# Optimization experiments

Hardware: AMD Instinct MI355X
Metric: run time of the kernel (lower is better)

The kernel has to match this reference:

```python
import jax, jax.numpy as jnp
import numpy as np
from jax import lax


def setup_inputs() -> dict:
    key = jax.random.key(0)
    ks = jax.random.split(key, 6)
    B, L, D, H, K = 32, 256, 16, 64, 5
    T = L - K + 1            # 252
    S = (T // 2) * H         # 8064
    return {
        "x": jax.random.normal(ks[0], (B, L, D), dtype=jnp.float32),
        "conv_w": jax.random.normal(ks[1], (D, H, K), dtype=jnp.float32) * 0.1,
        "conv_b": jax.random.normal(ks[2], (D, H), dtype=jnp.float32) * 0.1,
        "deconv_w": jax.random.normal(ks[3], (D, H, K), dtype=jnp.float32) * 0.1,
        "deconv_b": jax.random.normal(ks[4], (D,), dtype=jnp.float32) * 0.1,
        "W_attn": jax.random.normal(ks[5], (S, S), dtype=jnp.float32) * 0.01,
    }


def reference(x, conv_w, conv_b, deconv_w, deconv_b, W_attn):
    B, L, D = x.shape
    _, H, K = conv_w.shape
    T = L - K + 1
    P = T // 2
    S = P * H

    xt = jnp.transpose(x, (0, 2, 1))  # [B, D, L]
    # per-channel Conv1d(1->H) as one grouped conv: kernel [D*H, 1, K], groups=D
    y = lax.conv_general_dilated(
        xt, conv_w.reshape(D * H, 1, K), (1,), "VALID",
        dimension_numbers=("NCH", "OIH", "NCH"), feature_group_count=D,
    ) + conv_b.reshape(1, D * H, 1)
    y = jax.nn.relu(y)  # [B, D*H, T]

    # per-channel ConvTranspose1d(H->1) == full conv with flipped kernel, groups=D
    recon = lax.conv_general_dilated(
        y, deconv_w[..., ::-1], (1,), [(K - 1, K - 1)],
        dimension_numbers=("NCH", "OIH", "NCH"), feature_group_count=D,
    ) + deconv_b.reshape(1, D, 1)  # [B, D, L]

    # AvgPool1d(kernel=2, stride=2) then flatten(H, P) per channel
    pooled = y.reshape(B, D, H, P, 2).mean(axis=-1)  # [B, D, H, P]
    flat = pooled.reshape(B, D, S)                   # [B, D, S]

    main = flat[:, 0]        # [B, S]
    aux = flat[:, 1:]        # [B, D-1, S]

    # 'general' score: main . (aux @ W^T)  ==  (main @ W) . aux
    m = main @ W_attn                              # [B, S]
    scores = jnp.einsum("bt,bdt->bd", m, aux)      # [B, D-1]
    attn = jax.nn.softmax(scores, axis=-1)         # [B, D-1]
    weighted = jnp.einsum("bd,bds->bs", attn, aux)  # [B, S]

    out = jnp.concatenate([main[:, None, :], weighted[:, None, :]], axis=2)  # [B,1,2S]
    return out, attn[:, None, :], recon
```

## Files before the change

### kernel.cpp

```cpp
#include <hip/hip_runtime.h>
#include <math.h>

#define BB 32
#define LL 256
#define DD 16
#define HH 64
#define KK 5
#define TT 252
#define PP 126
#define SS 8064
#define NCHUNK 21
#define CHUNK 384
#define NKT 12

typedef __attribute__((ext_vector_type(8))) short bf16x8;
typedef __attribute__((ext_vector_type(4))) float f32x4;

__device__ __forceinline__ unsigned short f2bf(float f) {
  unsigned int u = __float_as_uint(f);
  u += 0x7FFFu + ((u >> 16) & 1u);
  return (unsigned short)(u >> 16);
}
__device__ __forceinline__ float bf2f(unsigned short h) {
  return __uint_as_float(((unsigned int)h) << 16);
}

__global__ __launch_bounds__(256) void k12_conv_recon(
    const float* __restrict__ x, const float* __restrict__ cw,
    const float* __restrict__ cb, const float* __restrict__ dw,
    const float* __restrict__ db, float* __restrict__ flat,
    unsigned short* __restrict__ mainH, unsigned short* __restrict__ mainL,
    float* __restrict__ recon) {
  __shared__ float ylds[HH * TT];
  __shared__ float xs[LL];
  __shared__ float cws[HH * KK];
  __shared__ float dws[HH * KK];
  __shared__ float cbs[HH];

  int bd = blockIdx.x;
  int b = bd / DD, d = bd % DD;
  int tid = threadIdx.x;

  xs[tid] = x[((size_t)b * LL + tid) * DD + d];
  for (int i = tid; i < HH * KK; i += 256) {
    cws[i] = cw[(size_t)d * HH * KK + i];
    dws[i] = dw[(size_t)d * HH * KK + i];
  }
  if (tid < HH) cbs[tid] = cb[d * HH + tid];
  __syncthreads();

  {
    int h = tid >> 2, a = tid & 3;
    int t0 = a * 63;
    float w0 = cws[h * KK + 0], w1 = cws[h * KK + 1], w2 = cws[h * KK + 2],
          w3 = cws[h * KK + 3], w4 = cws[h * KK + 4];
    float bias = cbs[h];
    float x0 = xs[t0], x1 = xs[t0 + 1], x2 = xs[t0 + 2], x3 = xs[t0 + 3],
          x4 = xs[t0 + 4];
    float* yrow = ylds + h * TT + t0;
    #pragma unroll 7
    for (int t = 0; t < 63; ++t) {
      float yv = fmaf(w4, x4, fmaf(w3, x3, fmaf(w2, x2, fmaf(w1, x1, fmaf(w0, x0, bias)))));
      yrow[t] = fmaxf(yv, 0.f);
      x0 = x1; x1 = x2; x2 = x3; x3 = x4;
      if (t < 62) x4 = xs[t0 + t + 5];
    }
  }
  __syncthreads();

  for (int i = tid; i < HH * PP; i += 256) {
    int h = i / PP, p = i - h * PP;
    float pooled = 0.5f * (ylds[h * TT + 2 * p] + ylds[h * TT + 2 * p + 1]);
    flat[(size_t)bd * SS + i] = pooled;
    if (d == 0) {
      unsigned short hb = f2bf(pooled);
      mainH[(size_t)b * SS + i] = hb;
      mainL[(size_t)b * SS + i] = f2bf(pooled - bf2f(hb));
    }
  }

  {
    int l = tid;
    float acc = db[d];
    for (int h = 0; h < HH; ++h) {
      const float* yl = ylds + h * TT;
      #pragma unroll
      for (int j = 0; j < KK; ++j) {
        int t = l - j;
        if (t >= 0 && t < TT) acc = fmaf(yl[t], dws[h * KK + j], acc);
      }
    }
    recon[(size_t)bd * LL + l] = acc;
  }
}

__global__ __launch_bounds__(256) void k3_mfma(
    const float* __restrict__ W, const unsigned short* __restrict__ mainH,
    const unsigned short* __restrict__ mainL, float* __restrict__ partial) {
  __shared__ unsigned short AH[2][1024];
  __shared__ unsigned short AL[2][1024];
  __shared__ unsigned short BH[2][4096];

  int tid = threadIdx.x;
  int chunk = blockIdx.y;
  int s0 = chunk * CHUNK;
  int cbase = blockIdx.x * 128;

  int lane = tid & 63;
  int wv = tid >> 6;
  int mr = wv & 1;
  int ctb = (wv >> 1) * 4;

  f32x4 c0 = {0.f, 0.f, 0.f, 0.f};
  f32x4 c1 = {0.f, 0.f, 0.f, 0.f};
  f32x4 c2 = {0.f, 0.f, 0.f, 0.f};
  f32x4 c3 = {0.f, 0.f, 0.f, 0.f};

  int sc2 = (tid & 63) * 2;
  int sg = tid >> 6;
  const float* wbase = W + (size_t)(s0 + sg * 8) * SS + cbase + sc2;

  int ab = tid >> 2, aq = tid & 3;
  size_t abase = (size_t)ab * SS + (size_t)(s0 + aq * 8);

  int aoff  = (lane >> 4) * 256 + ((lane & 15) + 16 * mr) * 8;
  int boff0 = (lane >> 4) * 1024 + (ctb * 16 + (lane & 15)) * 8;

  float2 e0, e1, e2, e3, e4, e5, e6, e7;
  float2 o0, o1, o2, o3, o4, o5, o6, o7;
  bf16x8 aEH, aEL, aOH, aOL;

#define LOADW(R0,R1,R2,R3,R4,R5,R6,R7, KT) {                          \
    const float* p_ = wbase + (size_t)(KT) * 32 * SS;                 \
    R0 = *(const float2*)(p_);                                        \
    R1 = *(const float2*)(p_ + (size_t)SS);                           \
    R2 = *(const float2*)(p_ + 2 * (size_t)SS);                       \
    R3 = *(const float2*)(p_ + 3 * (size_t)SS);                       \
    R4 = *(const float2*)(p_ + 4 * (size_t)SS);                       \
    R5 = *(const float2*)(p_ + 5 * (size_t)SS);                       \
    R6 = *(const float2*)(p_ + 6 * (size_t)SS);                       \
    R7 = *(const float2*)(p_ + 7 * (size_t)SS); }

#define LOADA(RH, RL, KT) if (tid < 128) {                            \
    RH = *(const bf16x8*)(mainH + abase + (KT) * 32);                 \
    RL = *(const bf16x8*)(mainL + abase + (KT) * 32); }

#define CVT1(F, J) {                                                  \
    h0[J] = (short)f2bf(F.x);                                         \
    h1[J] = (short)f2bf(F.y); }

#define CVTW(R0,R1,R2,R3,R4,R5,R6,R7, BUF) {                          \
    bf16x8 h0, h1;                                                    \
    CVT1(R0, 0) CVT1(R1, 1) CVT1(R2, 2) CVT1(R3, 3)                   \
    CVT1(R4, 4) CVT1(R5, 5) CVT1(R6, 6) CVT1(R7, 7)                   \
    *(bf16x8*)&BH[BUF][sg * 1024 + sc2 * 8]     = h0;                 \
    *(bf16x8*)&BH[BUF][sg * 1024 + sc2 * 8 + 8] = h1; }

#define WRITEA(RH, RL, BUF) if (tid < 128) {                          \
    *(bf16x8*)&AH[BUF][aq * 256 + ab * 8] = RH;                       \
    *(bf16x8*)&AL[BUF][aq * 256 + ab * 8] = RL; }

#define DOMFMA(BUF) {                                                 \
    bf16x8 ah  = *(const bf16x8*)&AH[BUF][aoff];                      \
    bf16x8 al  = *(const bf16x8*)&AL[BUF][aoff];                      \
    bf16x8 bh0 = *(const bf16x8*)&BH[BUF][boff0];                     \
    bf16x8 bh1 = *(const bf16x8*)&BH[BUF][boff0 + 128];               \
    bf16x8 bh2 = *(const bf16x8*)&BH[BUF][boff0 + 256];               \
    bf16x8 bh3 = *(const bf16x8*)&BH[BUF][boff0 + 384];               \
    c0 = __builtin_amdgcn_mfma_f32_16x16x32_bf16(ah, bh0, c0, 0, 0, 0); \
    c0 = __builtin_amdgcn_mfma_f32_16x16x32_bf16(al, bh0, c0, 0, 0, 0); \
    c1 = __builtin_amdgcn_mfma_f32_16x16x32_bf16(ah, bh1, c1, 0, 0, 0); \
    c1 = __builtin_amdgcn_mfma_f32_16x16x32_bf16(al, bh1, c1, 0, 0, 0); \
    c2 = __builtin_amdgcn_mfma_f32_16x16x32_bf16(ah, bh2, c2, 0, 0, 0); \
    c2 = __builtin_amdgcn_mfma_f32_16x16x32_bf16(al, bh2, c2, 0, 0, 0); \
    c3 = __builtin_amdgcn_mfma_f32_16x16x32_bf16(ah, bh3, c3, 0, 0, 0); \
    c3 = __builtin_amdgcn_mfma_f32_16x16x32_bf16(al, bh3, c3, 0, 0, 0); }

  LOADW(e0,e1,e2,e3,e4,e5,e6,e7, 0) LOADA(aEH, aEL, 0)
  CVTW(e0,e1,e2,e3,e4,e5,e6,e7, 0) WRITEA(aEH, aEL, 0)
  LOADW(o0,o1,o2,o3,o4,o5,o6,o7, 1) LOADA(aOH, aOL, 1)
  __syncthreads();

  #pragma unroll 1
  for (int kt = 0; kt < NKT; kt += 2) {
    if (kt + 2 < NKT) { LOADW(e0,e1,e2,e3,e4,e5,e6,e7, kt + 2) LOADA(aEH, aEL, kt + 2) }
    DOMFMA(0)
    CVTW(o0,o1,o2,o3,o4,o5,o6,o7, 1) WRITEA(aOH, aOL, 1)
    __syncthreads();
    if (kt + 3 < NKT) { LOADW(o0,o1,o2,o3,o4,o5,o6,o7, kt + 3) LOADA(aOH, aOL, kt + 3) }
    DOMFMA(1)
    if (kt + 2 < NKT) { CVTW(e0,e1,e2,e3,e4,e5,e6,e7, 0) WRITEA(aEH, aEL, 0) }
    __syncthreads();
  }

  int row0 = mr * 16 + (lane >> 4) * 4;
  int col0 = cbase + ctb * 16 + (lane & 15);
  float* pp = partial + ((size_t)chunk * BB + row0) * SS + col0;
  #pragma unroll
  for (int r = 0; r < 4; ++r) pp[(size_t)r * SS]      = c0[r];
  #pragma unroll
  for (int r = 0; r < 4; ++r) pp[(size_t)r * SS + 16] = c1[r];
  #pragma unroll
  for (int r = 0; r < 4; ++r) pp[(size_t)r * SS + 32] = c2[r];
  #pragma unroll
  for (int r = 0; r < 4; ++r) pp[(size_t)r * SS + 48] = c3[r];
#undef LOADW
#undef LOADA
#undef CVT1
#undef CVTW
#undef WRITEA
#undef DOMFMA
}

__global__ __launch_bounds__(256) void k3b_reduce(
    const float4* __restrict__ partial, float4* __restrict__ m) {
  int i = blockIdx.x * 256 + threadIdx.x;
  float4 s = make_float4(0.f, 0.f, 0.f, 0.f);
  #pragma unroll
  for (int c = 0; c < NCHUNK; ++c) {
    float4 v = partial[(size_t)c * (BB * SS / 4) + i];
    s.x += v.x; s.y += v.y; s.z += v.z; s.w += v.w;
  }
  m[i] = s;
}

__global__ __launch_bounds__(256) void k4_scores(
    const float* __restrict__ m, const float* __restrict__ flat,
    float* __restrict__ scores) {
  int bd = blockIdx.x;
  int b = bd / 15, dd = bd % 15;
  const float* mb = m + (size_t)b * SS;
  const float* ab = flat + ((size_t)b * DD + 1 + dd) * SS;
  float p = 0.f;
  for (int s = threadIdx.x; s < SS; s += 256) p = fmaf(mb[s], ab[s], p);
  #pragma unroll
  for (int o = 32; o; o >>= 1) p += __shfl_xor(p, o);
  __shared__ float red[4];
  if ((threadIdx.x & 63) == 0) red[threadIdx.x >> 6] = p;
  __syncthreads();
  if (threadIdx.x == 0) scores[bd] = red[0] + red[1] + red[2] + red[3];
}

__global__ __launch_bounds__(64) void k5_softmax(
    const float* __restrict__ scores, float* __restrict__ attn_out) {
  int b = blockIdx.x;
  int lane = threadIdx.x;
  float v = (lane < 15) ? scores[b * 15 + lane] : -INFINITY;
  float mx = v;
  #pragma unroll
  for (int o = 32; o; o >>= 1) mx = fmaxf(mx, __shfl_xor(mx, o));
  float e = (lane < 15) ? expf(v - mx) : 0.f;
  float sum = e;
  #pragma unroll
  for (int o = 32; o; o >>= 1) sum += __shfl_xor(sum, o);
  if (lane < 15) attn_out[b * 15 + lane] = e / sum;
}

__global__ __launch_bounds__(256) void k6_out(
    const float* __restrict__ flat, const float* __restrict__ attn,
    float* __restrict__ out) {
  int b = blockIdx.y;
  int s = blockIdx.x * 256 + threadIdx.x;
  if (s >= SS) return;
  const float* fb = flat + (size_t)b * DD * SS;
  out[(size_t)b * 2 * SS + s] = fb[s];
  float w = 0.f;
  #pragma unroll
  for (int d = 0; d < 15; ++d)
    w = fmaf(attn[b * 15 + d], fb[(size_t)(1 + d) * SS + s], w);
  out[(size_t)b * 2 * SS + SS + s] = w;
}

extern "C" void kernel_launch(void* const* d_in, const int* in_sizes, int n_in,
                              void* d_out, int out_size, void* d_ws, size_t ws_size,
                              hipStream_t stream) {
  const float* x        = (const float*)d_in[0];
  const float* conv_w   = (const float*)d_in[1];
  const float* conv_b   = (const float*)d_in[2];
  const float* deconv_w = (const float*)d_in[3];
  const float* deconv_b = (const float*)d_in[4];
  const float* W_attn   = (const float*)d_in[5];
  float* out = (float*)d_out;

  const size_t ATTN_OFF  = (size_t)BB * 2 * SS;
  const size_t RECON_OFF = ATTN_OFF + (size_t)BB * 15;

  float* ws      = (float*)d_ws;
  float* partial = ws;
  float* flat    = partial + (size_t)NCHUNK * BB * SS;
  unsigned short* mainH = (unsigned short*)(flat + (size_t)BB * DD * SS);
  unsigned short* mainL = mainH + (size_t)BB * SS;
  float* m       = (float*)(mainL + (size_t)BB * SS);
  float* scores  = m + (size_t)BB * SS;

  k12_conv_recon<<<dim3(BB * DD), dim3(256), 0, stream>>>(
      x, conv_w, conv_b, deconv_w, deconv_b, flat, mainH, mainL, out + RECON_OFF);

  k3_mfma<<<dim3(SS / 128, NCHUNK), dim3(256), 0, stream>>>(
      W_attn, mainH, mainL, partial);

  k3b_reduce<<<dim3((BB * SS / 4) / 256), dim3(256), 0, stream>>>(
      (const float4*)partial, (float4*)m);

  k4_scores<<<dim3(BB * 15), dim3(256), 0, stream>>>(m, flat, scores);

  k5_softmax<<<dim3(BB), dim3(64), 0, stream>>>(scores, out + ATTN_OFF);

  k6_out<<<dim3((SS + 255) / 256, BB), dim3(256), 0, stream>>>(
      flat, out + ATTN_OFF, out);
}
```

Measured before the change: 104.2 us.

## Fuse softmax into output kernel and rebalance split-K chunking of GEMV

The softmax kernel is removed. Every block of the output kernel now recomputes the 15-way softmax from the raw scores, and block 0 writes the attention weights. The split-K matmul moves from 21 chunks of 384 to 12 chunks of 672, with the K-loop reworked for an odd tile count. This cuts partial-sum traffic and the reduce cost but lowers grid parallelism for the matmul. The x load in the conv kernel also switches to a float4 read with lane selection.

```diff
diff --git a/kernel.cpp b/kernel.cpp
--- a/kernel.cpp
+++ b/kernel.cpp
@@ -9,9 +9,9 @@
 #define TT 252
 #define PP 126
 #define SS 8064
-#define NCHUNK 21
-#define CHUNK 384
-#define NKT 12
+#define NCHUNK 12
+#define CHUNK 672
+#define NKT 21
 
 typedef __attribute__((ext_vector_type(8))) short bf16x8;
 typedef __attribute__((ext_vector_type(4))) float f32x4;
@@ -41,7 +41,12 @@
   int b = bd / DD, d = bd % DD;
   int tid = threadIdx.x;
 
-  xs[tid] = x[((size_t)b * LL + tid) * DD + d];
+  {
+    float4 xv = *(const float4*)(x + ((size_t)b * LL + tid) * DD + (d & ~3));
+    int dl = d & 3;
+    float v = (dl == 0) ? xv.x : (dl == 1) ? xv.y : (dl == 2) ? xv.z : xv.w;
+    xs[tid] = v;
+  }
   for (int i = tid; i < HH * KK; i += 256) {
     cws[i] = cw[(size_t)d * HH * KK + i];
     dws[i] = dw[(size_t)d * HH * KK + i];
@@ -182,16 +187,19 @@
   __syncthreads();
 
   #pragma unroll 1
-  for (int kt = 0; kt < NKT; kt += 2) {
-    if (kt + 2 < NKT) { LOADW(e0,e1,e2,e3,e4,e5,e6,e7, kt + 2) LOADA(aEH, aEL, kt + 2) }
+  for (int kt = 0; kt < NKT - 1; kt += 2) {
+    LOADW(e0,e1,e2,e3,e4,e5,e6,e7, kt + 2) LOADA(aEH, aEL, kt + 2)
     DOMFMA(0)
     CVTW(o0,o1,o2,o3,o4,o5,o6,o7, 1) WRITEA(aOH, aOL, 1)
     __syncthreads();
-    if (kt + 3 < NKT) { LOADW(o0,o1,o2,o3,o4,o5,o6,o7, kt + 3) LOADA(aOH, aOL, kt + 3) }
+    if (kt + 3 < NKT) {
+      LOADW(o0,o1,o2,o3,o4,o5,o6,o7, kt + 3) LOADA(aOH, aOL, kt + 3)
+    }
     DOMFMA(1)
-    if (kt + 2 < NKT) { CVTW(e0,e1,e2,e3,e4,e5,e6,e7, 0) WRITEA(aEH, aEL, 0) }
+    CVTW(e0,e1,e2,e3,e4,e5,e6,e7, 0) WRITEA(aEH, aEL, 0)
     __syncthreads();
   }
+  DOMFMA(0)
 
   int row0 = mr * 16 + (lane >> 4) * 4;
   int col0 = cbase + ctb * 16 + (lane & 15);
@@ -241,33 +249,57 @@
   if (threadIdx.x == 0) scores[bd] = red[0] + red[1] + red[2] + red[3];
 }
 
-__global__ __launch_bounds__(64) void k5_softmax(
-    const float* __restrict__ scores, float* __restrict__ attn_out) {
-  int b = blockIdx.x;
-  int lane = threadIdx.x;
-  float v = (lane < 15) ? scores[b * 15 + lane] : -INFINITY;
-  float mx = v;
-  #pragma unroll
-  for (int o = 32; o; o >>= 1) mx = fmaxf(mx, __shfl_xor(mx, o));
-  float e = (lane < 15) ? expf(v - mx) : 0.f;
-  float sum = e;
-  #pragma unroll
-  for (int o = 32; o; o >>= 1) sum += __shfl_xor(sum, o);
-  if (lane < 15) attn_out[b * 15 + lane] = e / sum;
-}
-
 __global__ __launch_bounds__(256) void k6_out(
-    const float* __restrict__ flat, const float* __restrict__ attn,
-    float* __restrict__ out) {
+    const float* __restrict__ flat, const float* __restrict__ scores,
+    float* __restrict__ out, float* __restrict__ attn_out) {
   int b = blockIdx.y;
   int s = blockIdx.x * 256 + threadIdx.x;
+
+  float e0_, mx = -INFINITY;
+  float sc[1]; (void)sc;
+  float v0 = scores[b * 15 + 0], v1 = scores[b * 15 + 1], v2 = scores[b * 15 + 2],
+        v3 = scores[b * 15 + 3], v4 = scores[b * 15 + 4], v5 = scores[b * 15 + 5],
+        v6 = scores[b * 15 + 6], v7 = scores[b * 15 + 7], v8 = scores[b * 15 + 8],
+        v9 = scores[b * 15 + 9], v10 = scores[b * 15 + 10], v11 = scores[b * 15 + 11],
+        v12 = scores[b * 15 + 12], v13 = scores[b * 15 + 13], v14 = scores[b * 15 + 14];
+  mx = fmaxf(mx, v0);  mx = fmaxf(mx, v1);  mx = fmaxf(mx, v2);
+  mx = fmaxf(mx, v3);  mx = fmaxf(mx, v4);  mx = fmaxf(mx, v5);
+  mx = fmaxf(mx, v6);  mx = fmaxf(mx, v7);  mx = fmaxf(mx, v8);
+  mx = fmaxf(mx, v9);  mx = fmaxf(mx, v10); mx = fmaxf(mx, v11);
+  mx = fmaxf(mx, v12); mx = fmaxf(mx, v13); mx = fmaxf(mx, v14);
+  float a0 = expf(v0 - mx), a1 = expf(v1 - mx), a2 = expf(v2 - mx),
+        a3 = expf(v3 - mx), a4 = expf(v4 - mx), a5 = expf(v5 - mx),
+        a6 = expf(v6 - mx), a7 = expf(v7 - mx), a8 = expf(v8 - mx),
+        a9 = expf(v9 - mx), a10 = expf(v10 - mx), a11 = expf(v11 - mx),
+        a12 = expf(v12 - mx), a13 = expf(v13 - mx), a14 = expf(v14 - mx);
+  float sum = a0 + a1 + a2 + a3 + a4 + a5 + a6 + a7 + a8 + a9 + a10 + a11 +
+              a12 + a13 + a14;
+  float inv = 1.f / sum;
+  e0_ = inv; (void)e0_;
+
+  if (blockIdx.x == 0 && threadIdx.x < 15)
+    attn_out[b * 15 + threadIdx.x] =
+        expf(scores[b * 15 + threadIdx.x] - mx) * inv;
+
   if (s >= SS) return;
   const float* fb = flat + (size_t)b * DD * SS;
   out[(size_t)b * 2 * SS + s] = fb[s];
   float w = 0.f;
-  #pragma unroll
-  for (int d = 0; d < 15; ++d)
-    w = fmaf(attn[b * 15 + d], fb[(size_t)(1 + d) * SS + s], w);
+  w = fmaf(a0 * inv,  fb[(size_t)1 * SS + s], w);
+  w = fmaf(a1 * inv,  fb[(size_t)2 * SS + s], w);
+  w = fmaf(a2 * inv,  fb[(size_t)3 * SS + s], w);
+  w = fmaf(a3 * inv,  fb[(size_t)4 * SS + s], w);
+  w = fmaf(a4 * inv,  fb[(size_t)5 * SS + s], w);
+  w = fmaf(a5 * inv,  fb[(size_t)6 * SS + s], w);
+  w = fmaf(a6 * inv,  fb[(size_t)7 * SS + s], w);
+  w = fmaf(a7 * inv,  fb[(size_t)8 * SS + s], w);
+  w = fmaf(a8 * inv,  fb[(size_t)9 * SS + s], w);
+  w = fmaf(a9 * inv,  fb[(size_t)10 * SS + s], w);
+  w = fmaf(a10 * inv, fb[(size_t)11 * SS + s], w);
+  w = fmaf(a11 * inv, fb[(size_t)12 * SS + s], w);
+  w = fmaf(a12 * inv, fb[(size_t)13 * SS + s], w);
+  w = fmaf(a13 * inv, fb[(size_t)14 * SS + s], w);
+  w = fmaf(a14 * inv, fb[(size_t)15 * SS + s], w);
   out[(size_t)b * 2 * SS + SS + s] = w;
 }
 
@@ -304,8 +336,6 @@
 
   k4_scores<<<dim3(BB * 15), dim3(256), 0, stream>>>(m, flat, scores);
 
-  k5_softmax<<<dim3(BB), dim3(64), 0, stream>>>(scores, out + ATTN_OFF);
-
   k6_out<<<dim3((SS + 255) / 256, BB), dim3(256), 0, stream>>>(
-      flat, out + ATTN_OFF, out);
-}
+      flat, scores, out, out + ATTN_OFF);
+}
```

Measured after the change: 96.88 us. 7.1% less time.
